# Kernel optimization log

Hardware: AMD Instinct MI355X
Metric: run time of the kernel (lower is better)

The kernel has to match this reference:

```python
import jax, jax.numpy as jnp
import numpy as np
from jax import lax

N, E, IN, OUT, H, OH = 2048, 16384, 128, 128, 4, 8
NEG_SLOPE = 0.2

def symlog(v):
    return jnp.sign(v) * jnp.log1p(jnp.abs(v))

def setup_inputs() -> dict:
    key = jax.random.key(0)
    ks = jax.random.split(key, 16)
    x = jax.random.normal(ks[0], (N, IN), dtype=jnp.float32)
    onehot = jax.random.uniform(ks[1], (N, N), dtype=jnp.float32)
    src = jax.random.randint(ks[2], (E,), 0, N, dtype=jnp.int32)
    # guarantee no self loops (original removes them before adding its own)
    off = jax.random.randint(ks[3], (E,), 1, N, dtype=jnp.int32)
    dst = (src + off) % N
    s = 0.05
    lin_w = jax.random.normal(ks[4], (H * OUT, IN + OH), dtype=jnp.float32) * s
    att_l = jax.random.normal(ks[5], (1, H, OUT), dtype=jnp.float32) * s
    att_r = jax.random.normal(ks[6], (1, H, OUT), dtype=jnp.float32) * s
    bias = jnp.zeros((H * OUT,), dtype=jnp.float32)
    conv1_w = jax.random.normal(ks[7], (8, 1, 3), dtype=jnp.float32) * s
    conv1_b = jnp.zeros((8,), dtype=jnp.float32)
    conv2_w = jax.random.normal(ks[8], (16, 8, 3), dtype=jnp.float32) * s
    conv2_b = jnp.zeros((16,), dtype=jnp.float32)
    fc_w = jax.random.normal(ks[9], (OH, 16), dtype=jnp.float32) * s
    fc_b = jnp.zeros((OH,), dtype=jnp.float32)
    return {"x": x, "onehot": onehot, "src": src, "dst": dst,
            "lin_w": lin_w, "att_l": att_l, "att_r": att_r, "bias": bias,
            "conv1_w": conv1_w, "conv1_b": conv1_b, "conv2_w": conv2_w,
            "conv2_b": conv2_b, "fc_w": fc_w, "fc_b": fc_b}

def _forward(x, onehot, src, dst, lin_w, att_l, att_r, bias,
             conv1_w, conv1_b, conv2_w, conv2_b, fc_w, fc_b):
    n = x.shape[0]
    # --- one-hot conv pipeline: sort -> symlog -> Conv1d x2 -> avgpool -> Linear ---
    prep = symlog(jnp.sort(onehot, axis=-1))[:, None, :]          # [N,1,N]
    dn = ('NCH', 'OIH', 'NCH')
    h = lax.conv_general_dilated(prep, conv1_w, (1,), [(1, 1)], dimension_numbers=dn)
    h = jax.nn.relu(h + conv1_b[None, :, None])                    # [N,8,N]
    h = lax.conv_general_dilated(h, conv2_w, (1,), [(1, 1)], dimension_numbers=dn)
    h = jax.nn.relu(h + conv2_b[None, :, None])                    # [N,16,N]
    pooled = h.mean(axis=-1)                                       # AdaptiveAvgPool1d(1) -> [N,16]
    oh_feat = pooled @ fc_w.T + fc_b                               # [N,OH]
    # --- linear + per-head attention logits ---
    xh = (jnp.concatenate([x, oh_feat], axis=-1) @ lin_w.T).reshape(n, H, OUT)
    sa = (xh * att_l).sum(-1)                                      # [N,H]
    ra = (xh * att_r).sum(-1)
    # --- add self loops (input edges contain none) ---
    loop = jnp.arange(n, dtype=src.dtype)
    s_i = jnp.concatenate([src, loop])
    d_i = jnp.concatenate([dst, loop])
    # --- message: LeakyReLU attention * one-hot dot attention ---
    alpha = jax.nn.leaky_relu(sa[s_i] + ra[d_i], NEG_SLOPE)        # [E',H]
    send_oh = onehot[s_i]                                          # [E',N]
    dotatt = 1.0 / ((symlog(send_oh) * symlog(onehot[d_i])).sum(axis=1) + 1.0)
    alpha = alpha * dotatt[:, None]
    # --- segment softmax over receiving node ---
    amax = jax.ops.segment_max(alpha, d_i, num_segments=n)
    ex = jnp.exp(alpha - amax[d_i])
    den = jax.ops.segment_sum(ex, d_i, num_segments=n)
    alpha = ex / (den[d_i] + 1e-16)
    # --- weighted aggregate (scatter-sum) ---
    agg_x = jax.ops.segment_sum(xh[s_i] * alpha[:, :, None], d_i, num_segments=n)
    agg_oh = jax.ops.segment_sum(send_oh, d_i, num_segments=n)
    new_x = agg_x.reshape(n, H * OUT) + bias                       # concat heads + bias
    new_onehot = onehot + agg_oh                                   # one_hot_incay='add'
    return new_x, new_onehot

def reference(x, onehot, src, dst, lin_w, att_l, att_r, bias,
              conv1_w, conv1_b, conv2_w, conv2_b, fc_w, fc_b):
    return _forward(x, onehot, src, dst, lin_w, att_l, att_r, bias,
                    conv1_w, conv1_b, conv2_w, conv2_b, fc_w, fc_b)
```

## Files before the change

### kernel.cpp

```cpp
#include <hip/hip_runtime.h>
#include <math.h>

#define NN   2048
#define NE   16384
#define NET  (NE + NN)
#define INF_ 128
#define OUTF 128
#define NH   4
#define OHF  8
#define NEG_SLOPE 0.2f
#define CAP  512

__device__ __forceinline__ float symlogf_(float v) {
    float s = log1pf(fabsf(v));
    return v < 0.0f ? -s : s;
}

__global__ __launch_bounds__(256, 2) void k_sortconv(
    const float* __restrict__ onehot,
    const float* __restrict__ c1w, const float* __restrict__ c1b,
    const float* __restrict__ c2w, const float* __restrict__ c2b,
    const float* __restrict__ fcw, const float* __restrict__ fcb,
    float* __restrict__ slog, float* __restrict__ ohfeat) {
    __shared__ float vals[NN];
    __shared__ float red[64];
    __shared__ float pooled[16];
    const int t = threadIdx.x;
    const int r = blockIdx.x;
    const int b = t << 3;
    const float* row  = onehot + (size_t)r * NN;
    float*       srow = slog   + (size_t)r * NN;

    float4 lo = ((const float4*)row)[t * 2];
    float4 hi = ((const float4*)row)[t * 2 + 1];
    float v[8] = {lo.x, lo.y, lo.z, lo.w, hi.x, hi.y, hi.z, hi.w};
    {
        float4 s0, s1;
        s0.x = symlogf_(v[0]); s0.y = symlogf_(v[1]);
        s0.z = symlogf_(v[2]); s0.w = symlogf_(v[3]);
        s1.x = symlogf_(v[4]); s1.y = symlogf_(v[5]);
        s1.z = symlogf_(v[6]); s1.w = symlogf_(v[7]);
        ((float4*)srow)[t * 2]     = s0;
        ((float4*)srow)[t * 2 + 1] = s1;
    }

    auto cx = [](float& x, float& y, bool up) {
        float mn = fminf(x, y), mx = fmaxf(x, y);
        x = up ? mn : mx;
        y = up ? mx : mn;
    };

    cx(v[0], v[1], true);  cx(v[2], v[3], false);
    cx(v[4], v[5], true);  cx(v[6], v[7], false);
    cx(v[0], v[2], true);  cx(v[1], v[3], true);
    cx(v[4], v[6], false); cx(v[5], v[7], false);
    cx(v[0], v[1], true);  cx(v[2], v[3], true);
    cx(v[4], v[5], false); cx(v[6], v[7], false);
    {
        const bool u8 = ((t & 1) == 0);
        cx(v[0], v[4], u8); cx(v[1], v[5], u8); cx(v[2], v[6], u8); cx(v[3], v[7], u8);
        cx(v[0], v[2], u8); cx(v[1], v[3], u8); cx(v[4], v[6], u8); cx(v[5], v[7], u8);
        cx(v[0], v[1], u8); cx(v[2], v[3], u8); cx(v[4], v[5], u8); cx(v[6], v[7], u8);
    }

    for (int k = 16; k <= NN; k <<= 1) {
        const bool up = ((b & k) == 0);
        for (int j = k >> 1; j >= 8; j >>= 1) {
            const int pj = j >> 3;
            const bool keepmin = (((t & pj) == 0) == up);
            if (pj <= 32) {
                #pragma unroll
                for (int e = 0; e < 8; e++) {
                    float p = __shfl_xor(v[e], pj, 64);
                    v[e] = keepmin ? fminf(v[e], p) : fmaxf(v[e], p);
                }
            } else {
                __syncthreads();
                #pragma unroll
                for (int e = 0; e < 8; e++) vals[b + e] = v[e];
                __syncthreads();
                const int pb = (t ^ pj) << 3;
                #pragma unroll
                for (int e = 0; e < 8; e++) {
                    float p = vals[pb + e];
                    v[e] = keepmin ? fminf(v[e], p) : fmaxf(v[e], p);
                }
            }
        }
        cx(v[0], v[4], up); cx(v[1], v[5], up); cx(v[2], v[6], up); cx(v[3], v[7], up);
        cx(v[0], v[2], up); cx(v[1], v[3], up); cx(v[4], v[6], up); cx(v[5], v[7], up);
        cx(v[0], v[1], up); cx(v[2], v[3], up); cx(v[4], v[5], up); cx(v[6], v[7], up);
    }

    #pragma unroll
    for (int e = 0; e < 8; e++) v[e] = symlogf_(v[e]);

    __syncthreads();
    #pragma unroll
    for (int e = 0; e < 8; e++) vals[b + e] = v[e];
    __syncthreads();

    float vv[12];
    vv[0]  = (b - 2 >= 0) ? vals[b - 2] : 0.0f;
    vv[1]  = (b - 1 >= 0) ? vals[b - 1] : 0.0f;
    #pragma unroll
    for (int e = 0; e < 8; e++) vv[2 + e] = v[e];
    vv[10] = (b + 8 < NN) ? vals[b + 8] : 0.0f;
    vv[11] = (b + 9 < NN) ? vals[b + 9] : 0.0f;

    float h1c[10][8];
    #pragma unroll
    for (int m = 0; m < 10; m++) {
        const int q = b - 1 + m;
        const bool ok = (q >= 0) && (q < NN);
        const float xm = vv[m], xc = vv[m + 1], xp = vv[m + 2];
        #pragma unroll
        for (int c = 0; c < 8; c++) {
            float a = c1b[c];
            a = fmaf(c1w[c * 3 + 0], xm, a);
            a = fmaf(c1w[c * 3 + 1], xc, a);
            a = fmaf(c1w[c * 3 + 2], xp, a);
            h1c[m][c] = ok ? fmaxf(a, 0.0f) : 0.0f;
        }
    }

    float sums[16];
    #pragma unroll
    for (int ch = 0; ch < 16; ch++) {
        const float bb = c2b[ch];
        float acc = 0.0f;
        #pragma unroll
        for (int i = 0; i < 8; i++) {
            float a = bb;
            #pragma unroll
            for (int c = 0; c < 8; c++) {
                a = fmaf(c2w[ch * 24 + c * 3 + 0], h1c[i][c],     a);
                a = fmaf(c2w[ch * 24 + c * 3 + 1], h1c[i + 1][c], a);
                a = fmaf(c2w[ch * 24 + c * 3 + 2], h1c[i + 2][c], a);
            }
            acc += fmaxf(a, 0.0f);
        }
        sums[ch] = acc;
    }

    const int wave = t >> 6, lane = t & 63;
    #pragma unroll
    for (int c = 0; c < 16; c++)
        for (int o = 32; o; o >>= 1) sums[c] += __shfl_down(sums[c], o);
    if (lane == 0)
        #pragma unroll
        for (int c = 0; c < 16; c++) red[wave * 16 + c] = sums[c];
    __syncthreads();
    if (t < 16)
        pooled[t] = (red[t] + red[16 + t] + red[32 + t] + red[48 + t]) * (1.0f / NN);
    __syncthreads();
    if (t < OHF) {
        float a = fcb[t];
        #pragma unroll
        for (int c = 0; c < 16; c++) a = fmaf(fcw[t * 16 + c], pooled[c], a);
        ohfeat[r * OHF + t] = a;
    }
}

__global__ __launch_bounds__(256) void k_xh(
    const float* __restrict__ x, const float* __restrict__ ohf,
    const float* __restrict__ lin_w, float* __restrict__ xh) {
    const int n0 = blockIdx.x * 4;
    __shared__ float xin[4][136];
    const int tid = threadIdx.x;
    for (int i = tid; i < 4 * 136; i += 256) {
        int nn = i / 136, k = i - nn * 136;
        xin[nn][k] = (k < INF_) ? x[(size_t)(n0+nn)*INF_ + k]
                                : ohf[(n0+nn)*OHF + (k - INF_)];
    }
    __syncthreads();
    for (int o = tid; o < 512; o += 256) {
        const float4* wr4 = (const float4*)(lin_w + (size_t)o * 136);
        float a0 = 0, a1 = 0, a2 = 0, a3 = 0;
        for (int kk = 0; kk < 34; kk++) {
            float4 w = wr4[kk];
            int k = kk * 4;
            a0 += w.x*xin[0][k] + w.y*xin[0][k+1] + w.z*xin[0][k+2] + w.w*xin[0][k+3];
            a1 += w.x*xin[1][k] + w.y*xin[1][k+1] + w.z*xin[1][k+2] + w.w*xin[1][k+3];
            a2 += w.x*xin[2][k] + w.y*xin[2][k+1] + w.z*xin[2][k+2] + w.w*xin[2][k+3];
            a3 += w.x*xin[3][k] + w.y*xin[3][k+1] + w.z*xin[3][k+2] + w.w*xin[3][k+3];
        }
        xh[(size_t)(n0+0)*512 + o] = a0;
        xh[(size_t)(n0+1)*512 + o] = a1;
        xh[(size_t)(n0+2)*512 + o] = a2;
        xh[(size_t)(n0+3)*512 + o] = a3;
    }
}

__global__ __launch_bounds__(256) void k_attn(
    const float* __restrict__ xh, const float* __restrict__ att_l,
    const float* __restrict__ att_r, float* __restrict__ sa,
    float* __restrict__ ra) {
    const int n = blockIdx.x;
    const int tid = threadIdx.x, wave = tid >> 6, lane = tid & 63;
    const float* xr = xh + (size_t)n * 512 + wave * 128;
    float v0 = xr[lane], v1 = xr[lane + 64];
    float pl = v0 * att_l[wave*128 + lane] + v1 * att_l[wave*128 + lane + 64];
    float pr = v0 * att_r[wave*128 + lane] + v1 * att_r[wave*128 + lane + 64];
    for (int o = 32; o; o >>= 1) { pl += __shfl_down(pl, o); pr += __shfl_down(pr, o); }
    if (lane == 0) { sa[n*4 + wave] = pl; ra[n*4 + wave] = pr; }
}

__global__ void k_count(const int* __restrict__ dst, int* __restrict__ deg) {
    int e = blockIdx.x * 256 + threadIdx.x;
    if (e < NET) {
        int d = (e < NE) ? dst[e] : (e - NE);
        atomicAdd(&deg[d], 1);
    }
}

__global__ __launch_bounds__(256) void k_scan(
    const int* __restrict__ deg, int* __restrict__ csr_off,
    int* __restrict__ csr_pos) {
    __shared__ int tot[256];
    __shared__ int base[257];
    const int t = threadIdx.x;
    int loc[8], s = 0;
    for (int k = 0; k < 8; k++) { loc[k] = deg[t*8 + k]; s += loc[k]; }
    tot[t] = s;
    __syncthreads();
    if (t == 0) {
        int acc = 0;
        for (int i = 0; i < 256; i++) { base[i] = acc; acc += tot[i]; }
        base[256] = acc;
    }
    __syncthreads();
    int b = base[t];
    for (int k = 0; k < 8; k++) {
        csr_off[t*8 + k] = b;
        csr_pos[t*8 + k] = b;
        b += loc[k];
    }
    if (t == 0) csr_off[NN] = base[256];
}

__global__ void k_fill(const int* __restrict__ dst, int* __restrict__ csr_pos,
                       int* __restrict__ csr_e) {
    int e = blockIdx.x * 256 + threadIdx.x;
    if (e < NET) {
        int d = (e < NE) ? dst[e] : (e - NE);
        int pos = atomicAdd(&csr_pos[d], 1);
        csr_e[pos] = e;
    }
}

__global__ __launch_bounds__(256) void k_alpha(
    const int* __restrict__ src, const int* __restrict__ dst,
    const float* __restrict__ slog, const float* __restrict__ sa,
    const float* __restrict__ ra, float* __restrict__ alpha) {
    const int e = blockIdx.x;
    int s, d;
    if (e < NE) { s = src[e]; d = dst[e]; } else { s = d = e - NE; }
    const int tid = threadIdx.x;
    const float4* A = (const float4*)(slog + (size_t)s * NN);
    const float4* B = (const float4*)(slog + (size_t)d * NN);
    float4 a0 = A[tid*2], a1 = A[tid*2 + 1];
    float4 b0 = B[tid*2], b1 = B[tid*2 + 1];
    float p = a0.x*b0.x + a0.y*b0.y + a0.z*b0.z + a0.w*b0.w
            + a1.x*b1.x + a1.y*b1.y + a1.z*b1.z + a1.w*b1.w;
    for (int o = 32; o; o >>= 1) p += __shfl_down(p, o);
    __shared__ float ps[4];
    const int wave = tid >> 6, lane = tid & 63;
    if (lane == 0) ps[wave] = p;
    __syncthreads();
    if (tid == 0) {
        float dot  = ps[0] + ps[1] + ps[2] + ps[3];
        float datt = 1.0f / (dot + 1.0f);
        float4 out;
        float* po = (float*)&out;
        for (int h = 0; h < 4; h++) {
            float a = sa[s*4 + h] + ra[d*4 + h];
            a = (a >= 0.0f) ? a : NEG_SLOPE * a;
            po[h] = a * datt;
        }
        *(float4*)(alpha + (size_t)e * 4) = out;
    }
}

__global__ __launch_bounds__(256) void k_soft_aggx(
    const int* __restrict__ src, const int* __restrict__ csr_off,
    const int* __restrict__ csr_e, const float* __restrict__ alpha,
    const float* __restrict__ xh, const float* __restrict__ bias,
    float* __restrict__ out_x) {
    const int d = blockIdx.x;
    const int begin = csr_off[d];
    int deg = csr_off[d + 1] - begin;
    if (deg > CAP) deg = CAP;
    __shared__ float wls[CAP * 4];
    __shared__ int   sls[CAP];
    const int tid = threadIdx.x;
    for (int t = tid; t < deg; t += 256) {
        int e = csr_e[begin + t];
        sls[t] = (e < NE) ? src[e] : (e - NE);
        float4 a = *(const float4*)(alpha + (size_t)e * 4);
        wls[t*4 + 0] = a.x; wls[t*4 + 1] = a.y;
        wls[t*4 + 2] = a.z; wls[t*4 + 3] = a.w;
    }
    __syncthreads();
    const int wave = tid >> 6, lane = tid & 63;
    if (wave < 4) {
        float m = -3.4e38f;
        for (int t = lane; t < deg; t += 64) m = fmaxf(m, wls[t*4 + wave]);
        for (int o = 32; o; o >>= 1) m = fmaxf(m, __shfl_down(m, o));
        m = __shfl(m, 0);
        float s = 0.0f;
        for (int t = lane; t < deg; t += 64) {
            float ex = expf(wls[t*4 + wave] - m);
            wls[t*4 + wave] = ex;
            s += ex;
        }
        for (int o = 32; o; o >>= 1) s += __shfl_down(s, o);
        s = __shfl(s, 0);
        float inv = 1.0f / (s + 1e-16f);
        for (int t = lane; t < deg; t += 64) wls[t*4 + wave] *= inv;
    }
    __syncthreads();
    for (int ho = tid; ho < 512; ho += 256) {
        const int h = ho >> 7;
        float acc = 0.0f;
        for (int t = 0; t < deg; t++)
            acc += wls[t*4 + h] * xh[(size_t)sls[t] * 512 + ho];
        out_x[(size_t)d * 512 + ho] = acc + bias[ho];
    }
}

__global__ __launch_bounds__(256) void k_aggoh(
    const float* __restrict__ onehot, const int* __restrict__ src,
    const int* __restrict__ csr_off, const int* __restrict__ csr_e,
    float* __restrict__ out_oh) {
    const int d = blockIdx.x;
    const int begin = csr_off[d], end = csr_off[d + 1];
    const int tid = threadIdx.x;
    const float4* own = (const float4*)(onehot + (size_t)d * NN);
    float4 A = own[tid], B = own[tid + 256];
    for (int p = begin; p < end; p++) {
        int e = csr_e[p];
        int s = (e < NE) ? src[e] : (e - NE);
        const float4* r4 = (const float4*)(onehot + (size_t)s * NN);
        float4 u = r4[tid], v = r4[tid + 256];
        A.x += u.x; A.y += u.y; A.z += u.z; A.w += u.w;
        B.x += v.x; B.y += v.y; B.z += v.z; B.w += v.w;
    }
    float4* o4 = (float4*)(out_oh + (size_t)d * NN);
    o4[tid] = A; o4[tid + 256] = B;
}

extern "C" void kernel_launch(void* const* d_in, const int* in_sizes, int n_in,
                              void* d_out, int out_size, void* d_ws, size_t ws_size,
                              hipStream_t stream) {
    const float* x      = (const float*)d_in[0];
    const float* onehot = (const float*)d_in[1];
    const int*   src    = (const int*)d_in[2];
    const int*   dst    = (const int*)d_in[3];
    const float* lin_w  = (const float*)d_in[4];
    const float* att_l  = (const float*)d_in[5];
    const float* att_r  = (const float*)d_in[6];
    const float* bias   = (const float*)d_in[7];
    const float* c1w    = (const float*)d_in[8];
    const float* c1b    = (const float*)d_in[9];
    const float* c2w    = (const float*)d_in[10];
    const float* c2b    = (const float*)d_in[11];
    const float* fcw    = (const float*)d_in[12];
    const float* fcb    = (const float*)d_in[13];

    float* out_x  = (float*)d_out;
    float* out_oh = out_x + (size_t)NN * (NH * OUTF);

    float* ws    = (float*)d_ws;
    float* slog  = ws;
    float* xh    = slog + (size_t)NN * NN;
    float* ohf   = xh   + (size_t)NN * 512;
    float* sa    = ohf  + (size_t)NN * OHF;
    float* ra    = sa   + (size_t)NN * NH;
    float* alpha = ra   + (size_t)NN * NH;
    int* deg     = (int*)(alpha + (size_t)NET * 4);
    int* csr_off = deg + NN;
    int* csr_pos = csr_off + NN + 1;
    int* csr_e   = csr_pos + NN;

    hipMemsetAsync(deg, 0, NN * sizeof(int), stream);
    k_sortconv<<<NN, 256, 0, stream>>>(onehot, c1w, c1b, c2w, c2b, fcw, fcb, slog, ohf);
    k_count<<<(NET + 255) / 256, 256, 0, stream>>>(dst, deg);
    k_scan<<<1, 256, 0, stream>>>(deg, csr_off, csr_pos);
    k_fill<<<(NET + 255) / 256, 256, 0, stream>>>(dst, csr_pos, csr_e);
    k_xh<<<NN / 4, 256, 0, stream>>>(x, ohf, lin_w, xh);
    k_attn<<<NN, 256, 0, stream>>>(xh, att_l, att_r, sa, ra);
    k_alpha<<<NET, 256, 0, stream>>>(src, dst, slog, sa, ra, alpha);
    k_soft_aggx<<<NN, 256, 0, stream>>>(src, csr_off, csr_e, alpha, xh, bias, out_x);
    k_aggoh<<<NN, 256, 0, stream>>>(onehot, src, csr_off, csr_e, out_oh);
}
```

Baseline: 294.4 us.

## Fuse attention projection into xh kernel, restructure conv pipeline and scan

Several independent changes land together. symlog now uses the fast __logf intrinsic instead of log1pf, which changes precision for small inputs. The bitonic sort's shared-memory exchange moves to a structure-of-arrays layout to reduce bank conflicts. The conv1/conv2 stage computes conv1 columns on the fly in a rolling three-column window, with halo values passed by shuffles instead of a shared-memory round-trip, which cuts register pressure. The attention dot products are fused into k_xh so the separate k_attn launch and its reread of xh are gone, and the serial single-thread scan is replaced with a wave shuffle scan.

```diff
diff --git a/kernel.cpp b/kernel.cpp
--- a/kernel.cpp
+++ b/kernel.cpp
@@ -12,8 +12,7 @@
 #define CAP  512
 
 __device__ __forceinline__ float symlogf_(float v) {
-    float s = log1pf(fabsf(v));
-    return v < 0.0f ? -s : s;
+    return copysignf(__logf(1.0f + fabsf(v)), v);
 }
 
 __global__ __launch_bounds__(256, 2) void k_sortconv(
@@ -22,12 +21,15 @@
     const float* __restrict__ c2w, const float* __restrict__ c2b,
     const float* __restrict__ fcw, const float* __restrict__ fcb,
     float* __restrict__ slog, float* __restrict__ ohfeat) {
-    __shared__ float vals[NN];
+    __shared__ float soa[NN];
+    __shared__ float bndL[4][2];
+    __shared__ float bndR[4][2];
     __shared__ float red[64];
     __shared__ float pooled[16];
     const int t = threadIdx.x;
     const int r = blockIdx.x;
     const int b = t << 3;
+    const int wave = t >> 6, lane = t & 63;
     const float* row  = onehot + (size_t)r * NN;
     float*       srow = slog   + (size_t)r * NN;
 
@@ -77,12 +79,12 @@
             } else {
                 __syncthreads();
                 #pragma unroll
-                for (int e = 0; e < 8; e++) vals[b + e] = v[e];
+                for (int e = 0; e < 8; e++) soa[e * 256 + t] = v[e];
                 __syncthreads();
-                const int pb = (t ^ pj) << 3;
+                const int pt = t ^ pj;
                 #pragma unroll
                 for (int e = 0; e < 8; e++) {
-                    float p = vals[pb + e];
+                    float p = soa[e * 256 + pt];
                     v[e] = keepmin ? fminf(v[e], p) : fmaxf(v[e], p);
                 }
             }
@@ -96,54 +98,75 @@
     for (int e = 0; e < 8; e++) v[e] = symlogf_(v[e]);
 
     __syncthreads();
-    #pragma unroll
-    for (int e = 0; e < 8; e++) vals[b + e] = v[e];
-    __syncthreads();
-
-    float vv[12];
-    vv[0]  = (b - 2 >= 0) ? vals[b - 2] : 0.0f;
-    vv[1]  = (b - 1 >= 0) ? vals[b - 1] : 0.0f;
-    #pragma unroll
-    for (int e = 0; e < 8; e++) vv[2 + e] = v[e];
-    vv[10] = (b + 8 < NN) ? vals[b + 8] : 0.0f;
-    vv[11] = (b + 9 < NN) ? vals[b + 9] : 0.0f;
-
-    float h1c[10][8];
-    #pragma unroll
-    for (int m = 0; m < 10; m++) {
-        const int q = b - 1 + m;
-        const bool ok = (q >= 0) && (q < NN);
-        const float xm = vv[m], xc = vv[m + 1], xp = vv[m + 2];
-        #pragma unroll
-        for (int c = 0; c < 8; c++) {
-            float a = c1b[c];
-            a = fmaf(c1w[c * 3 + 0], xm, a);
-            a = fmaf(c1w[c * 3 + 1], xc, a);
-            a = fmaf(c1w[c * 3 + 2], xp, a);
-            h1c[m][c] = ok ? fmaxf(a, 0.0f) : 0.0f;
-        }
-    }
-
+    if (lane == 63) { bndL[wave][0] = v[6]; bndL[wave][1] = v[7]; }
+    if (lane == 0)  { bndR[wave][0] = v[0]; bndR[wave][1] = v[1]; }
+    __syncthreads();
+    float vm2 = __shfl_up(v[6], 1, 64);
+    float vm1 = __shfl_up(v[7], 1, 64);
+    float vp8 = __shfl_down(v[0], 1, 64);
+    float vp9 = __shfl_down(v[1], 1, 64);
+    if (lane == 0) {
+        vm2 = wave ? bndL[wave - 1][0] : 0.0f;
+        vm1 = wave ? bndL[wave - 1][1] : 0.0f;
+    }
+    if (lane == 63) {
+        vp8 = (wave < 3) ? bndR[wave + 1][0] : 0.0f;
+        vp9 = (wave < 3) ? bndR[wave + 1][1] : 0.0f;
+    }
+
+    float vin[12];
+    vin[0] = vm2; vin[1] = vm1;
+    #pragma unroll
+    for (int e = 0; e < 8; e++) vin[2 + e] = v[e];
+    vin[10] = vp8; vin[11] = vp9;
+
+    float cols[3][8];
     float sums[16];
     #pragma unroll
-    for (int ch = 0; ch < 16; ch++) {
-        const float bb = c2b[ch];
-        float acc = 0.0f;
-        #pragma unroll
-        for (int i = 0; i < 8; i++) {
-            float a = bb;
+    for (int c = 0; c < 16; c++) sums[c] = 0.0f;
+
+#define MKCOL(I, COL)                                                         \
+    {                                                                         \
+        const float xm = vin[(I)], xc = vin[(I) + 1], xp = vin[(I) + 2];      \
+        _Pragma("unroll")                                                     \
+        for (int c = 0; c < 8; c++) {                                         \
+            float a = fmaf(c1w[c * 3 + 2], xp,                                \
+                      fmaf(c1w[c * 3 + 1], xc,                                \
+                      fmaf(c1w[c * 3 + 0], xm, c1b[c])));                     \
+            (COL)[c] = fmaxf(a, 0.0f);                                        \
+        }                                                                     \
+        if ((I) == 0) {                                                       \
+            if (t == 0) { _Pragma("unroll")                                   \
+                for (int c = 0; c < 8; c++) (COL)[c] = 0.0f; }                \
+        }                                                                     \
+        if ((I) == 9) {                                                       \
+            if (t == 255) { _Pragma("unroll")                                 \
+                for (int c = 0; c < 8; c++) (COL)[c] = 0.0f; }                \
+        }                                                                     \
+    }
+
+    MKCOL(0, cols[0]);
+    MKCOL(1, cols[1]);
+    #pragma unroll
+    for (int ip = 0; ip < 8; ip++) {
+        MKCOL(ip + 2, cols[(ip + 2) % 3]);
+        const float* cA = cols[ip % 3];
+        const float* cB = cols[(ip + 1) % 3];
+        const float* cC = cols[(ip + 2) % 3];
+        #pragma unroll
+        for (int ch = 0; ch < 16; ch++) {
+            float a = c2b[ch];
             #pragma unroll
             for (int c = 0; c < 8; c++) {
-                a = fmaf(c2w[ch * 24 + c * 3 + 0], h1c[i][c],     a);
-                a = fmaf(c2w[ch * 24 + c * 3 + 1], h1c[i + 1][c], a);
-                a = fmaf(c2w[ch * 24 + c * 3 + 2], h1c[i + 2][c], a);
+                a = fmaf(c2w[ch * 24 + c * 3 + 0], cA[c], a);
+                a = fmaf(c2w[ch * 24 + c * 3 + 1], cB[c], a);
+                a = fmaf(c2w[ch * 24 + c * 3 + 2], cC[c], a);
             }
-            acc += fmaxf(a, 0.0f);
+            sums[ch] += fmaxf(a, 0.0f);
         }
-        sums[ch] = acc;
-    }
-
-    const int wave = t >> 6, lane = t & 63;
+    }
+#undef MKCOL
+
     #pragma unroll
     for (int c = 0; c < 16; c++)
         for (int o = 32; o; o >>= 1) sums[c] += __shfl_down(sums[c], o);
@@ -164,17 +187,29 @@
 
 __global__ __launch_bounds__(256) void k_xh(
     const float* __restrict__ x, const float* __restrict__ ohf,
-    const float* __restrict__ lin_w, float* __restrict__ xh) {
+    const float* __restrict__ lin_w, const float* __restrict__ att_l,
+    const float* __restrict__ att_r, float* __restrict__ xh,
+    float* __restrict__ sa, float* __restrict__ ra) {
     const int n0 = blockIdx.x * 4;
     __shared__ float xin[4][136];
+    __shared__ float part[4][16];
     const int tid = threadIdx.x;
+    const int wave = tid >> 6, lane = tid & 63;
     for (int i = tid; i < 4 * 136; i += 256) {
         int nn = i / 136, k = i - nn * 136;
         xin[nn][k] = (k < INF_) ? x[(size_t)(n0+nn)*INF_ + k]
                                 : ohf[(n0+nn)*OHF + (k - INF_)];
     }
     __syncthreads();
-    for (int o = tid; o < 512; o += 256) {
+    float accl[2][4], accr[2][4];
+    #pragma unroll
+    for (int g = 0; g < 2; g++)
+        #pragma unroll
+        for (int n = 0; n < 4; n++) { accl[g][n] = 0.0f; accr[g][n] = 0.0f; }
+
+    #pragma unroll
+    for (int g = 0; g < 2; g++) {
+        const int o = tid + g * 256;
         const float4* wr4 = (const float4*)(lin_w + (size_t)o * 136);
         float a0 = 0, a1 = 0, a2 = 0, a3 = 0;
         for (int kk = 0; kk < 34; kk++) {
@@ -189,21 +224,37 @@
         xh[(size_t)(n0+1)*512 + o] = a1;
         xh[(size_t)(n0+2)*512 + o] = a2;
         xh[(size_t)(n0+3)*512 + o] = a3;
-    }
-}
-
-__global__ __launch_bounds__(256) void k_attn(
-    const float* __restrict__ xh, const float* __restrict__ att_l,
-    const float* __restrict__ att_r, float* __restrict__ sa,
-    float* __restrict__ ra) {
-    const int n = blockIdx.x;
-    const int tid = threadIdx.x, wave = tid >> 6, lane = tid & 63;
-    const float* xr = xh + (size_t)n * 512 + wave * 128;
-    float v0 = xr[lane], v1 = xr[lane + 64];
-    float pl = v0 * att_l[wave*128 + lane] + v1 * att_l[wave*128 + lane + 64];
-    float pr = v0 * att_r[wave*128 + lane] + v1 * att_r[wave*128 + lane + 64];
-    for (int o = 32; o; o >>= 1) { pl += __shfl_down(pl, o); pr += __shfl_down(pr, o); }
-    if (lane == 0) { sa[n*4 + wave] = pl; ra[n*4 + wave] = pr; }
+        const float al = att_l[o], ar = att_r[o];
+        accl[g][0] = fmaf(a0, al, accl[g][0]); accr[g][0] = fmaf(a0, ar, accr[g][0]);
+        accl[g][1] = fmaf(a1, al, accl[g][1]); accr[g][1] = fmaf(a1, ar, accr[g][1]);
+        accl[g][2] = fmaf(a2, al, accl[g][2]); accr[g][2] = fmaf(a2, ar, accr[g][2]);
+        accl[g][3] = fmaf(a3, al, accl[g][3]); accr[g][3] = fmaf(a3, ar, accr[g][3]);
+    }
+    #pragma unroll
+    for (int g = 0; g < 2; g++)
+        #pragma unroll
+        for (int n = 0; n < 4; n++)
+            for (int o = 32; o; o >>= 1) {
+                accl[g][n] += __shfl_down(accl[g][n], o);
+                accr[g][n] += __shfl_down(accr[g][n], o);
+            }
+    if (lane == 0) {
+        #pragma unroll
+        for (int g = 0; g < 2; g++)
+            #pragma unroll
+            for (int n = 0; n < 4; n++) {
+                part[wave][n * 4 + g * 2 + 0] = accl[g][n];
+                part[wave][n * 4 + g * 2 + 1] = accr[g][n];
+            }
+    }
+    __syncthreads();
+    if (tid < 32) {
+        const int n = tid >> 3, rem = tid & 7, h = rem >> 1, lr = rem & 1;
+        const int g = h >> 1, wp = (h & 1) * 2;
+        const float val = part[wp][n * 4 + g * 2 + lr] + part[wp + 1][n * 4 + g * 2 + lr];
+        if (lr == 0) sa[(n0 + n) * 4 + h] = val;
+        else         ra[(n0 + n) * 4 + h] = val;
+    }
 }
 
 __global__ void k_count(const int* __restrict__ dst, int* __restrict__ deg) {
@@ -217,26 +268,29 @@
 __global__ __launch_bounds__(256) void k_scan(
     const int* __restrict__ deg, int* __restrict__ csr_off,
     int* __restrict__ csr_pos) {
-    __shared__ int tot[256];
-    __shared__ int base[257];
-    const int t = threadIdx.x;
+    __shared__ int wsum[4];
+    const int t = threadIdx.x, wave = t >> 6, lane = t & 63;
     int loc[8], s = 0;
+    #pragma unroll
     for (int k = 0; k < 8; k++) { loc[k] = deg[t*8 + k]; s += loc[k]; }
-    tot[t] = s;
-    __syncthreads();
-    if (t == 0) {
-        int acc = 0;
-        for (int i = 0; i < 256; i++) { base[i] = acc; acc += tot[i]; }
-        base[256] = acc;
-    }
-    __syncthreads();
-    int b = base[t];
+    int x = s;
+    for (int o = 1; o < 64; o <<= 1) {
+        int u = __shfl_up(x, o, 64);
+        if (lane >= o) x += u;
+    }
+    if (lane == 63) wsum[wave] = x;
+    __syncthreads();
+    int off = 0;
+    #pragma unroll
+    for (int w = 0; w < 4; w++) if (w < wave) off += wsum[w];
+    int base = off + x - s;
+    #pragma unroll
     for (int k = 0; k < 8; k++) {
-        csr_off[t*8 + k] = b;
-        csr_pos[t*8 + k] = b;
-        b += loc[k];
-    }
-    if (t == 0) csr_off[NN] = base[256];
+        csr_off[t*8 + k] = base;
+        csr_pos[t*8 + k] = base;
+        base += loc[k];
+    }
+    if (t == 255) csr_off[NN] = off + x;
 }
 
 __global__ void k_fill(const int* __restrict__ dst, int* __restrict__ csr_pos,
@@ -388,8 +442,7 @@
     k_count<<<(NET + 255) / 256, 256, 0, stream>>>(dst, deg);
     k_scan<<<1, 256, 0, stream>>>(deg, csr_off, csr_pos);
     k_fill<<<(NET + 255) / 256, 256, 0, stream>>>(dst, csr_pos, csr_e);
-    k_xh<<<NN / 4, 256, 0, stream>>>(x, ohf, lin_w, xh);
-    k_attn<<<NN, 256, 0, stream>>>(xh, att_l, att_r, sa, ra);
+    k_xh<<<NN / 4, 256, 0, stream>>>(x, ohf, lin_w, att_l, att_r, xh, sa, ra);
     k_alpha<<<NET, 256, 0, stream>>>(src, dst, slog, sa, ra, alpha);
     k_soft_aggx<<<NN, 256, 0, stream>>>(src, csr_off, csr_e, alpha, xh, bias, out_x);
     k_aggoh<<<NN, 256, 0, stream>>>(onehot, src, csr_off, csr_e, out_oh);
```

Result: no change. 298.7 us (+1.4%).
